# Kernel optimization log

Measured on AMD Instinct MI355X. Metric: run time of the kernel, lower is better.

The kernel has to match this reference:

```python
import jax, jax.numpy as jnp
import numpy as np

N_Q, N_X, N_Z = 1024, 512, 512
N_PER = N_Q + N_X + N_Z        # 2048 nodes per graph
B = 16                          # graphs per batch
DEG = 16                        # avg in/out degree
E_PER = N_PER * DEG
N = B * N_PER                   # 32768 total nodes
E = B * E_PER                   # 524288 total edges
HID, HEADS, L = 128, 4, 3
DH = HID // HEADS               # 32 per-head dim
EPS = 1e-5


def setup_inputs() -> dict:
    key = jax.random.key(0)
    ks = jax.random.split(key, 10)
    # one-hot node-type features (qubit / X-stab / Z-stab), tiled over batch
    sn = jnp.zeros((N_PER, 3), jnp.float32)
    sn = sn.at[:N_Q, 0].set(1.0).at[N_Q:N_Q + N_X, 1].set(1.0).at[N_Q + N_X:, 2].set(1.0)
    x = jnp.tile(sn, (B, 1))  # [N,3]
    # random sparse edges, graph-local then offset (mimics dense_to_sparse + Batch)
    src = jax.random.randint(ks[0], (B, E_PER), 0, N_PER)
    dst = jax.random.randint(ks[1], (B, E_PER), 0, N_PER)
    off = (jnp.arange(B) * N_PER)[:, None]
    edge_src = (src + off).reshape(-1).astype(jnp.int32)
    edge_dst = (dst + off).reshape(-1).astype(jnp.int32)
    seg = jnp.repeat(jnp.arange(B, dtype=jnp.int32), N_PER)  # graph id per node
    s = 0.05
    return dict(
        x=x, edge_src=edge_src, edge_dst=edge_dst, seg=seg,
        in_w=jax.random.normal(ks[2], (3, HID)) * s, in_b=jnp.zeros((HID,)),
        qw=jax.random.normal(ks[3], (L, HID, HID)) * s, qb=jnp.zeros((L, HID)),
        kw=jax.random.normal(ks[4], (L, HID, HID)) * s, kb=jnp.zeros((L, HID)),
        vw=jax.random.normal(ks[5], (L, HID, HID)) * s, vb=jnp.zeros((L, HID)),
        sw=jax.random.normal(ks[6], (L, HID, HID)) * s, sb=jnp.zeros((L, HID)),
        fw=jax.random.normal(ks[7], (L, HID, HID)) * s, fb=jnp.zeros((L, HID)),
        ln_g=jnp.ones((L, HID)), ln_b=jnp.zeros((L, HID)),
    )


def _layer_norm(h, g, b):
    mu = jnp.mean(h, axis=-1, keepdims=True)
    var = jnp.mean(jnp.square(h - mu), axis=-1, keepdims=True)
    return (h - mu) * jax.lax.rsqrt(var + EPS) * g + b


def reference(x, edge_src, edge_dst, seg, in_w, in_b, qw, qb, kw, kb, vw, vb,
              sw, sb, fw, fb, ln_g, ln_b):
    scale = 1.0 / jnp.sqrt(jnp.float32(DH))
    h = x @ in_w + in_b  # [N,HID]
    for i in range(L):
        h_res = h
        # TransformerConv: per-edge multi-head attention (softmax over in-neighbors)
        q = (h @ qw[i] + qb[i]).reshape(N, HEADS, DH)
        k = (h @ kw[i] + kb[i]).reshape(N, HEADS, DH)
        v = (h @ vw[i] + vb[i]).reshape(N, HEADS, DH)
        logits = jnp.einsum('ehd,ehd->eh', q[edge_dst], k[edge_src]) * scale  # [E,H]
        m = jax.ops.segment_max(logits, edge_dst, num_segments=N)             # [N,H]
        e = jnp.exp(logits - m[edge_dst])
        z = jax.ops.segment_sum(e, edge_dst, num_segments=N)                  # [N,H]
        alpha = e / z[edge_dst]
        agg = jax.ops.segment_sum(alpha[:, :, None] * v[edge_src], edge_dst,
                                  num_segments=N).reshape(N, HID)
        h = agg + h @ sw[i] + sb[i]        # root/skip linear (root_weight=True)
        # dropout is a no-op in eval mode
        h = h + jax.nn.relu(h @ fw[i] + fb[i])   # FFN residual
        h = h + h_res                            # outer residual
        h = jax.nn.relu(_layer_norm(h, ln_g[i], ln_b[i]))
    # global_mean_pool over graphs
    tot = jax.ops.segment_sum(h, seg, num_segments=B)                       # [B,HID]
    cnt = jax.ops.segment_sum(jnp.ones((N, 1), h.dtype), seg, num_segments=B)
    return tot / cnt
```

## Files before the change

### kernel.cpp

```cpp
#include <hip/hip_runtime.h>
#include <hip/hip_bf16.h>

#define N_TOT 32768
#define E_TOT 524288
#define HID 128
#define B_GR 16
#define NPER 2048
#define LAYERS 3
#define EPSLN 1e-5f
#define ELLW 64

typedef float f4 __attribute__((ext_vector_type(4)));
typedef float f2 __attribute__((ext_vector_type(2)));
typedef short bf16x8 __attribute__((ext_vector_type(8)));
typedef unsigned short u16x4 __attribute__((ext_vector_type(4)));

__device__ __forceinline__ unsigned short f2bf_rne(float x) {
    unsigned u = __float_as_uint(x);
    unsigned r = (u + 0x7FFFu + ((u >> 16) & 1u)) >> 16;
    return (unsigned short)r;
}

__device__ __forceinline__ void unpack8(uint4 w, float* f) {
    f[0] = __uint_as_float(w.x << 16); f[1] = __uint_as_float(w.x & 0xFFFF0000u);
    f[2] = __uint_as_float(w.y << 16); f[3] = __uint_as_float(w.y & 0xFFFF0000u);
    f[4] = __uint_as_float(w.z << 16); f[5] = __uint_as_float(w.z & 0xFFFF0000u);
    f[6] = __uint_as_float(w.w << 16); f[7] = __uint_as_float(w.w & 0xFFFF0000u);
}

__global__ __launch_bounds__(256) void k_zp(const float* __restrict__ qw, const float* __restrict__ kw,
                                            const float* __restrict__ vw, const float* __restrict__ sw,
                                            const float* __restrict__ fw, unsigned short* __restrict__ wt,
                                            int* __restrict__ cursor) {
    if (blockIdx.x < 960) {
        int mid = blockIdx.x >> 6;
        int within = (blockIdx.x & 63) * 256 + threadIdx.x;
        int l = mid / 5, t = mid % 5;
        const float* src = (t == 0 ? qw : t == 1 ? kw : t == 2 ? vw : t == 3 ? sw : fw) + l * HID * HID;
        int c = within >> 7;
        int kk = within & 127;
        int k = kk ^ ((c & 7) << 3);
        wt[mid * HID * HID + c * HID + kk] = f2bf_rne(src[k * HID + c]);
    } else {
        int i = (blockIdx.x - 960) * 256 + threadIdx.x;
        reinterpret_cast<int4*>(cursor)[i] = int4{0, 0, 0, 0};
    }
}

__global__ __launch_bounds__(256) void k_scatter_ell(const int* __restrict__ src, const int* __restrict__ dst,
                                                     int* __restrict__ cursor, int* __restrict__ ell) {
    int e = blockIdx.x * 256 + threadIdx.x;
    if (e < E_TOT) {
        int d = dst[e];
        int pos = atomicAdd(&cursor[d], 1);
        if (pos < ELLW) ell[d * ELLW + pos] = src[e];
    }
}

__device__ __forceinline__ void stage_A(const float* __restrict__ A, int r0,
                                        unsigned short (*A_lds)[HID], int tid) {
    #pragma unroll
    for (int p = 0; p < 8; ++p) {
        int idx = p * 256 + tid;
        int row = idx >> 5;
        int k0 = (idx & 31) * 4;
        f4 v = reinterpret_cast<const f4*>(A + (size_t)r0 * HID)[idx];
        u16x4 b = {f2bf_rne(v.x), f2bf_rne(v.y), f2bf_rne(v.z), f2bf_rne(v.w)};
        *reinterpret_cast<u16x4*>(&A_lds[row][k0 ^ ((row & 7) << 3)]) = b;
    }
}

#define GEMM_COMPUTE(acc, AL)                                                               \
    {                                                                                       \
        _Pragma("unroll")                                                                   \
        for (int ks = 0; ks < 4; ++ks) {                                                    \
            bf16x8 a0 = *reinterpret_cast<const bf16x8*>(                                   \
                &AL[wm * 32 + lr][(ks * 32 + lg * 8) ^ swz]);                               \
            bf16x8 a1 = *reinterpret_cast<const bf16x8*>(                                   \
                &AL[wm * 32 + 16 + lr][(ks * 32 + lg * 8) ^ swz]);                          \
            _Pragma("unroll")                                                               \
            for (int n = 0; n < 4; ++n) {                                                   \
                bf16x8 b = *reinterpret_cast<const bf16x8*>(                                \
                    &W_lds[wn * 64 + n * 16 + lr][(ks * 32 + lg * 8) ^ swz]);               \
                acc[0][n] = __builtin_amdgcn_mfma_f32_16x16x32_bf16(a0, b, acc[0][n], 0, 0, 0); \
                acc[1][n] = __builtin_amdgcn_mfma_f32_16x16x32_bf16(a1, b, acc[1][n], 0, 0, 0); \
            }                                                                               \
        }                                                                                   \
    }

__global__ __launch_bounds__(256) void k_init_qkv(const float* __restrict__ x,
                                                  const float* __restrict__ in_w,
                                                  const float* __restrict__ in_b,
                                                  const unsigned short* __restrict__ wl,
                                                  const float* __restrict__ qb, const float* __restrict__ kb,
                                                  const float* __restrict__ vb,
                                                  float* __restrict__ h,
                                                  unsigned short* __restrict__ oq, unsigned short* __restrict__ ok,
                                                  unsigned short* __restrict__ ov) {
    __shared__ unsigned short A_lds[64][HID];
    __shared__ unsigned short W_lds[HID][HID];
    int tid = threadIdx.x;
    int r0 = blockIdx.x * 64;
    int lane = tid & 63, w = tid >> 6;
    int wm = w >> 1, wn = w & 1;
    int lr = lane & 15, lg = lane >> 4;
    int swz = (lane & 7) << 3;

    #pragma unroll
    for (int p = 0; p < 8; ++p) {
        int idx = p * 256 + tid;
        int row = idx >> 5;
        int k0 = (idx & 31) * 4;
        int n = r0 + row;
        float x0 = x[n * 3 + 0], x1 = x[n * 3 + 1], x2 = x[n * 3 + 2];
        f4 o;
        #pragma unroll
        for (int i = 0; i < 4; ++i) {
            int c = k0 + i;
            o[i] = x0 * in_w[c] + x1 * in_w[HID + c] + x2 * in_w[2 * HID + c] + in_b[c];
        }
        reinterpret_cast<f4*>(h + (size_t)r0 * HID)[idx] = o;
        u16x4 b = {f2bf_rne(o[0]), f2bf_rne(o[1]), f2bf_rne(o[2]), f2bf_rne(o[3])};
        *reinterpret_cast<u16x4*>(&A_lds[row][k0 ^ ((row & 7) << 3)]) = b;
    }

    const float* biases[3] = {qb, kb, vb};
    unsigned short* outs[3] = {oq, ok, ov};
    #pragma unroll
    for (int t = 0; t < 3; ++t) {
        const unsigned short* Wp = wl + t * HID * HID;
        #pragma unroll
        for (int p = 0; p < 8; ++p) {
            int idx = p * 256 + tid;
            reinterpret_cast<f4*>(&W_lds[0][0])[idx] = reinterpret_cast<const f4*>(Wp)[idx];
        }
        __syncthreads();
        f4 acc[2][4];
        #pragma unroll
        for (int m = 0; m < 2; ++m)
            #pragma unroll
            for (int n = 0; n < 4; ++n) acc[m][n] = f4{0, 0, 0, 0};
        GEMM_COMPUTE(acc, A_lds);
        #pragma unroll
        for (int n = 0; n < 4; ++n) {
            int col = wn * 64 + n * 16 + lr;
            float bs = biases[t][col];
            #pragma unroll
            for (int m = 0; m < 2; ++m) {
                #pragma unroll
                for (int r = 0; r < 4; ++r) {
                    int row = r0 + wm * 32 + m * 16 + lg * 4 + r;
                    outs[t][(size_t)row * HID + col] = f2bf_rne(acc[m][n][r] + bs);
                }
            }
        }
        __syncthreads();
    }
}

__global__ __launch_bounds__(256) void k_attn4(const unsigned short* __restrict__ qb16,
                                               const unsigned short* __restrict__ kb16,
                                               const unsigned short* __restrict__ vb16,
                                               const int* __restrict__ deg,
                                               const int* __restrict__ ell,
                                               float* __restrict__ outagg) {
    int bid = blockIdx.x;
    int xcd = bid & 7;
    int chunk = bid >> 3;
    int g2 = xcd + 8 * (chunk >> 9);
    int nb = g2 * 512 + (chunk & 511);
    int n = nb * 4 + (threadIdx.x >> 6);

    int lane = threadIdx.x & 63;
    int g = lane >> 4, l = lane & 15;
    int dg = deg[n];
    if (dg > ELLW) dg = ELLW;
    const int base = n * ELLW;
    const float scale = 0.17677669529663687f;

    float qf[8];
    {
        uint4 qw = *reinterpret_cast<const uint4*>(&qb16[(size_t)n * HID + l * 8]);
        unpack8(qw, qf);
        #pragma unroll
        for (int c = 0; c < 8; ++c) qf[c] *= scale;
    }

    float z = 0.f;
    float a[8] = {0, 0, 0, 0, 0, 0, 0, 0};
    int nit = (dg + 3) >> 2;
    if (nit > 0) {
        int j = g;
        bool val = j < dg;
        int sj = ell[base + (val ? j : 0)];
        uint4 kw = *reinterpret_cast<const uint4*>(&kb16[(size_t)sj * HID + l * 8]);
        uint4 vw = *reinterpret_cast<const uint4*>(&vb16[(size_t)sj * HID + l * 8]);
        for (int it = 0; it < nit; ++it) {
            int jn = j + 4;
            bool valn = jn < dg;
            int sn = ell[base + (valn ? jn : 0)];
            uint4 kwn = *reinterpret_cast<const uint4*>(&kb16[(size_t)sn * HID + l * 8]);
            uint4 vwn = *reinterpret_cast<const uint4*>(&vb16[(size_t)sn * HID + l * 8]);
            float kf[8]; unpack8(kw, kf);
            float d = qf[0] * kf[0] + qf[1] * kf[1] + qf[2] * kf[2] + qf[3] * kf[3] +
                      qf[4] * kf[4] + qf[5] * kf[5] + qf[6] * kf[6] + qf[7] * kf[7];
            d += __shfl_xor(d, 1);
            d += __shfl_xor(d, 2);
            float p = val ? __expf(d) : 0.f;
            z += p;
            float vf[8]; unpack8(vw, vf);
            #pragma unroll
            for (int c = 0; c < 8; ++c) a[c] += p * vf[c];
            kw = kwn; vw = vwn; j = jn; val = valn;
        }
    }
    #pragma unroll
    for (int off = 16; off <= 32; off <<= 1) {
        z += __shfl_xor(z, off);
        #pragma unroll
        for (int c = 0; c < 8; ++c) a[c] += __shfl_xor(a[c], off);
    }
    if (g == 0) {
        float inv = (z > 0.f) ? 1.f / z : 0.f;
        f4 o0 = {a[0] * inv, a[1] * inv, a[2] * inv, a[3] * inv};
        f4 o1 = {a[4] * inv, a[5] * inv, a[6] * inv, a[7] * inv};
        f4* op = reinterpret_cast<f4*>(&outagg[(size_t)n * HID + l * 8]);
        op[0] = o0; op[1] = o1;
    }
}

template <bool QKV>
__global__ __launch_bounds__(256) void k_fused(const float* __restrict__ h,
                                               const unsigned short* __restrict__ wsf,
                                               const float* __restrict__ sb,
                                               const float* __restrict__ fb,
                                               const float* __restrict__ agg,
                                               const float* __restrict__ gma,
                                               const float* __restrict__ beta,
                                               float* __restrict__ out,
                                               const unsigned short* __restrict__ wqkv,
                                               const float* __restrict__ qb2,
                                               const float* __restrict__ kb2,
                                               const float* __restrict__ vb2,
                                               unsigned short* __restrict__ oq,
                                               unsigned short* __restrict__ ok,
                                               unsigned short* __restrict__ ov) {
    __shared__ __align__(16) char smem[50432];
    unsigned short (*A_lds)[HID] = reinterpret_cast<unsigned short (*)[HID]>(smem);
    unsigned short (*W_lds)[HID] = reinterpret_cast<unsigned short (*)[HID]>(smem + 16384);
    float (*T)[133] = reinterpret_cast<float (*)[133]>(smem + 16384);

    int tid = threadIdx.x;
    int r0 = blockIdx.x * 64;
    int lane = tid & 63, w = tid >> 6;
    int wm = w >> 1, wn = w & 1;
    int lr = lane & 15, lg = lane >> 4;
    int swz = (lane & 7) << 3;

    stage_A(h, r0, A_lds, tid);
    #pragma unroll
    for (int p = 0; p < 8; ++p) {
        int idx = p * 256 + tid;
        reinterpret_cast<f4*>(&W_lds[0][0])[idx] = reinterpret_cast<const f4*>(wsf)[idx];
    }
    __syncthreads();
    f4 acc[2][4];
    #pragma unroll
    for (int m = 0; m < 2; ++m)
        #pragma unroll
        for (int n = 0; n < 4; ++n) acc[m][n] = f4{0, 0, 0, 0};
    GEMM_COMPUTE(acc, A_lds);
    __syncthreads();

    #pragma unroll
    for (int n = 0; n < 4; ++n) {
        int col = wn * 64 + n * 16 + lr;
        float bs = sb[col];
        #pragma unroll
        for (int m = 0; m < 2; ++m) {
            #pragma unroll
            for (int r = 0; r < 4; ++r) {
                int rl = wm * 32 + m * 16 + lg * 4 + r;
                float v = acc[m][n][r] + bs + agg[(size_t)(r0 + rl) * HID + col];
                acc[m][n][r] = v;
                A_lds[rl][col ^ ((rl & 7) << 3)] = f2bf_rne(v);
            }
        }
    }
    #pragma unroll
    for (int p = 0; p < 8; ++p) {
        int idx = p * 256 + tid;
        reinterpret_cast<f4*>(&W_lds[0][0])[idx] = reinterpret_cast<const f4*>(wsf + HID * HID)[idx];
    }
    __syncthreads();
    f4 acc2[2][4];
    #pragma unroll
    for (int m = 0; m < 2; ++m)
        #pragma unroll
        for (int n = 0; n < 4; ++n) acc2[m][n] = f4{0, 0, 0, 0};
    GEMM_COMPUTE(acc2, A_lds);
    __syncthreads();

    #pragma unroll
    for (int n = 0; n < 4; ++n) {
        int col = wn * 64 + n * 16 + lr;
        float bs = fb[col];
        #pragma unroll
        for (int m = 0; m < 2; ++m) {
            #pragma unroll
            for (int r = 0; r < 4; ++r) {
                int rl = wm * 32 + m * 16 + lg * 4 + r;
                float t = acc[m][n][r] + fmaxf(acc2[m][n][r] + bs, 0.f) +
                          h[(size_t)(r0 + rl) * HID + col];
                T[rl][col] = t;
            }
        }
    }
    __syncthreads();

    int row = tid >> 2, qd = tid & 3;
    float s = 0.f, ss = 0.f;
    #pragma unroll 8
    for (int cc = 0; cc < 32; ++cc) {
        int c = (cc + qd * 8) & 31;
        float x = T[row][qd * 32 + c];
        s += x; ss += x * x;
    }
    s += __shfl_xor(s, 1);  s += __shfl_xor(s, 2);
    ss += __shfl_xor(ss, 1); ss += __shfl_xor(ss, 2);
    float mu = s * (1.f / 128.f);
    float var = ss * (1.f / 128.f) - mu * mu;
    float rsq = rsqrtf(fmaxf(var, 0.f) + EPSLN);
    int rswz = (row & 7) << 3;
    #pragma unroll
    for (int c4 = 0; c4 < 8; ++c4) {
        int cb = ((c4 + qd * 2) & 7) * 4;
        int col = qd * 32 + cb;
        f4 o;
        #pragma unroll
        for (int i = 0; i < 4; ++i) {
            float x = T[row][col + i];
            float y = (x - mu) * rsq * gma[col + i] + beta[col + i];
            o[i] = fmaxf(y, 0.f);
        }
        *reinterpret_cast<f4*>(&out[(size_t)(r0 + row) * HID + col]) = o;
        if (QKV) {
            u16x4 b = {f2bf_rne(o[0]), f2bf_rne(o[1]), f2bf_rne(o[2]), f2bf_rne(o[3])};
            *reinterpret_cast<u16x4*>(&A_lds[row][col ^ rswz]) = b;
        }
    }

    if (QKV) {
        __syncthreads();
        const float* biases[3] = {qb2, kb2, vb2};
        unsigned short* outs[3] = {oq, ok, ov};
        #pragma unroll
        for (int t = 0; t < 3; ++t) {
            const unsigned short* Wp = wqkv + t * HID * HID;
            #pragma unroll
            for (int p = 0; p < 8; ++p) {
                int idx = p * 256 + tid;
                reinterpret_cast<f4*>(&W_lds[0][0])[idx] = reinterpret_cast<const f4*>(Wp)[idx];
            }
            __syncthreads();
            f4 acc3[2][4];
            #pragma unroll
            for (int m = 0; m < 2; ++m)
                #pragma unroll
                for (int n = 0; n < 4; ++n) acc3[m][n] = f4{0, 0, 0, 0};
            GEMM_COMPUTE(acc3, A_lds);
            #pragma unroll
            for (int n = 0; n < 4; ++n) {
                int col = wn * 64 + n * 16 + lr;
                float bs = biases[t][col];
                #pragma unroll
                for (int m = 0; m < 2; ++m) {
                    #pragma unroll
                    for (int r = 0; r < 4; ++r) {
                        int rw = r0 + wm * 32 + m * 16 + lg * 4 + r;
                        outs[t][(size_t)rw * HID + col] = f2bf_rne(acc3[m][n][r] + bs);
                    }
                }
            }
            __syncthreads();
        }
    }
}

__global__ __launch_bounds__(128) void k_pool1(const float* __restrict__ h, float* __restrict__ partial) {
    int g = blockIdx.x >> 4, chunk = blockIdx.x & 15;
    int c = threadIdx.x;
    int n0 = g * NPER + chunk * 128;
    float s = 0.f;
    #pragma unroll 4
    for (int i = 0; i < 128; ++i) s += h[(size_t)(n0 + i) * HID + c];
    partial[(size_t)blockIdx.x * HID + c] = s;
}

__global__ __launch_bounds__(128) void k_pool2(const float* __restrict__ partial, float* __restrict__ out) {
    int g = blockIdx.x;
    int c = threadIdx.x;
    float s = 0.f;
    #pragma unroll
    for (int i = 0; i < 16; ++i) s += partial[(size_t)(g * 16 + i) * HID + c];
    out[g * HID + c] = s * (1.f / NPER);
}

extern "C" void kernel_launch(void* const* d_in, const int* in_sizes, int n_in,
                              void* d_out, int out_size, void* d_ws, size_t ws_size,
                              hipStream_t stream) {
    const float* x    = (const float*)d_in[0];
    const int*   esrc = (const int*)d_in[1];
    const int*   edst = (const int*)d_in[2];
    const float* in_w = (const float*)d_in[4];
    const float* in_b = (const float*)d_in[5];
    const float* qw   = (const float*)d_in[6];
    const float* qb   = (const float*)d_in[7];
    const float* kw   = (const float*)d_in[8];
    const float* kb   = (const float*)d_in[9];
    const float* vw   = (const float*)d_in[10];
    const float* vb   = (const float*)d_in[11];
    const float* sw   = (const float*)d_in[12];
    const float* sb   = (const float*)d_in[13];
    const float* fw   = (const float*)d_in[14];
    const float* fb   = (const float*)d_in[15];
    const float* ln_g = (const float*)d_in[16];
    const float* ln_b = (const float*)d_in[17];
    float* out = (float*)d_out;

    const size_t NH = (size_t)N_TOT * HID;
    float* h     = (float*)d_ws;
    float* t_buf = h + NH;
    float* partial = h + 2 * NH;
    unsigned short* qb16 = (unsigned short*)(partial + 256 * HID);
    unsigned short* kb16 = qb16 + NH;
    unsigned short* vb16 = kb16 + NH;
    unsigned short* wt   = vb16 + NH;
    int* cursor = (int*)(wt + 15 * HID * HID);
    int* ell    = cursor + N_TOT;

    k_zp<<<992, 256, 0, stream>>>(qw, kw, vw, sw, fw, wt, cursor);
    k_scatter_ell<<<E_TOT / 256, 256, 0, stream>>>(esrc, edst, cursor, ell);
    k_init_qkv<<<N_TOT / 64, 256, 0, stream>>>(x, in_w, in_b, wt, qb, kb, vb,
                                               h, qb16, kb16, vb16);

    for (int l = 0; l < LAYERS; ++l) {
        const unsigned short* wt_l = wt + (size_t)l * 5 * HID * HID;
        k_attn4<<<N_TOT / 4, 256, 0, stream>>>(qb16, kb16, vb16, cursor, ell, t_buf);
        if (l + 1 < LAYERS) {
            const unsigned short* wt_n = wt + (size_t)(l + 1) * 5 * HID * HID;
            k_fused<true><<<N_TOT / 64, 256, 0, stream>>>(
                h, wt_l + 3 * HID * HID, sb + (size_t)l * HID, fb + (size_t)l * HID,
                t_buf, ln_g + (size_t)l * HID, ln_b + (size_t)l * HID, h,
                wt_n, qb + (size_t)(l + 1) * HID, kb + (size_t)(l + 1) * HID,
                vb + (size_t)(l + 1) * HID, qb16, kb16, vb16);
        } else {
            k_fused<false><<<N_TOT / 64, 256, 0, stream>>>(
                h, wt_l + 3 * HID * HID, sb + (size_t)l * HID, fb + (size_t)l * HID,
                t_buf, ln_g + (size_t)l * HID, ln_b + (size_t)l * HID, h,
                nullptr, nullptr, nullptr, nullptr, nullptr, nullptr, nullptr);
        }
    }
    k_pool1<<<B_GR * 16, 128, 0, stream>>>(h, partial);
    k_pool2<<<B_GR, 128, 0, stream>>>(partial, out);
}
```

Measured before the change: 190.3 us.

## Interleave K/V, bf16 aggregates, 16-bit ELL indices, fold scale and pooling into kernels

```diff
diff --git a/kernel.cpp b/kernel.cpp
--- a/kernel.cpp
+++ b/kernel.cpp
@@ -9,9 +9,9 @@
 #define LAYERS 3
 #define EPSLN 1e-5f
 #define ELLW 64
+#define SCALE 0.17677669529663687f
 
 typedef float f4 __attribute__((ext_vector_type(4)));
-typedef float f2 __attribute__((ext_vector_type(2)));
 typedef short bf16x8 __attribute__((ext_vector_type(8)));
 typedef unsigned short u16x4 __attribute__((ext_vector_type(4)));
 
@@ -19,6 +19,10 @@
     unsigned u = __float_as_uint(x);
     unsigned r = (u + 0x7FFFu + ((u >> 16) & 1u)) >> 16;
     return (unsigned short)r;
+}
+
+__device__ __forceinline__ float bf2f(unsigned short u) {
+    return __uint_as_float(((unsigned)u) << 16);
 }
 
 __device__ __forceinline__ void unpack8(uint4 w, float* f) {
@@ -31,7 +35,7 @@
 __global__ __launch_bounds__(256) void k_zp(const float* __restrict__ qw, const float* __restrict__ kw,
                                             const float* __restrict__ vw, const float* __restrict__ sw,
                                             const float* __restrict__ fw, unsigned short* __restrict__ wt,
-                                            int* __restrict__ cursor) {
+                                            int* __restrict__ cursor, float* __restrict__ outz) {
     if (blockIdx.x < 960) {
         int mid = blockIdx.x >> 6;
         int within = (blockIdx.x & 63) * 256 + threadIdx.x;
@@ -40,20 +44,25 @@
         int c = within >> 7;
         int kk = within & 127;
         int k = kk ^ ((c & 7) << 3);
-        wt[mid * HID * HID + c * HID + kk] = f2bf_rne(src[k * HID + c]);
-    } else {
+        float sc = (t == 0) ? SCALE : 1.0f;
+        wt[mid * HID * HID + c * HID + kk] = f2bf_rne(src[k * HID + c] * sc);
+    } else if (blockIdx.x < 992) {
         int i = (blockIdx.x - 960) * 256 + threadIdx.x;
         reinterpret_cast<int4*>(cursor)[i] = int4{0, 0, 0, 0};
+    } else {
+        f4 z4 = {0.f, 0.f, 0.f, 0.f};
+        reinterpret_cast<f4*>(outz)[threadIdx.x * 2] = z4;
+        reinterpret_cast<f4*>(outz)[threadIdx.x * 2 + 1] = z4;
     }
 }
 
 __global__ __launch_bounds__(256) void k_scatter_ell(const int* __restrict__ src, const int* __restrict__ dst,
-                                                     int* __restrict__ cursor, int* __restrict__ ell) {
+                                                     int* __restrict__ cursor, unsigned short* __restrict__ ell) {
     int e = blockIdx.x * 256 + threadIdx.x;
     if (e < E_TOT) {
         int d = dst[e];
         int pos = atomicAdd(&cursor[d], 1);
-        if (pos < ELLW) ell[d * ELLW + pos] = src[e];
+        if (pos < ELLW) ell[d * ELLW + pos] = (unsigned short)src[e];
     }
 }
 
@@ -88,6 +97,26 @@
         }                                                                                   \
     }
 
+#define QKV_EPILOGUE(ACC, T_IDX)                                                            \
+    {                                                                                       \
+        _Pragma("unroll")                                                                   \
+        for (int n = 0; n < 4; ++n) {                                                       \
+            int col = wn * 64 + n * 16 + lr;                                                \
+            float bs = biases[T_IDX][col];                                                  \
+            if (T_IDX == 0) bs *= SCALE;                                                    \
+            unsigned short* outp = (T_IDX == 0) ? oq : okv + ((T_IDX == 2) ? 128 : 0);      \
+            const size_t stride = (T_IDX == 0) ? HID : 256;                                 \
+            _Pragma("unroll")                                                               \
+            for (int m = 0; m < 2; ++m) {                                                   \
+                _Pragma("unroll")                                                           \
+                for (int r = 0; r < 4; ++r) {                                               \
+                    int row = r0 + wm * 32 + m * 16 + lg * 4 + r;                           \
+                    outp[(size_t)row * stride + col] = f2bf_rne(ACC[m][n][r] + bs);         \
+                }                                                                           \
+            }                                                                               \
+        }                                                                                   \
+    }
+
 __global__ __launch_bounds__(256) void k_init_qkv(const float* __restrict__ x,
                                                   const float* __restrict__ in_w,
                                                   const float* __restrict__ in_b,
@@ -95,8 +124,8 @@
                                                   const float* __restrict__ qb, const float* __restrict__ kb,
                                                   const float* __restrict__ vb,
                                                   float* __restrict__ h,
-                                                  unsigned short* __restrict__ oq, unsigned short* __restrict__ ok,
-                                                  unsigned short* __restrict__ ov) {
+                                                  unsigned short* __restrict__ oq,
+                                                  unsigned short* __restrict__ okv) {
     __shared__ unsigned short A_lds[64][HID];
     __shared__ unsigned short W_lds[HID][HID];
     int tid = threadIdx.x;
@@ -125,7 +154,6 @@
     }
 
     const float* biases[3] = {qb, kb, vb};
-    unsigned short* outs[3] = {oq, ok, ov};
     #pragma unroll
     for (int t = 0; t < 3; ++t) {
         const unsigned short* Wp = wl + t * HID * HID;
@@ -141,29 +169,16 @@
             #pragma unroll
             for (int n = 0; n < 4; ++n) acc[m][n] = f4{0, 0, 0, 0};
         GEMM_COMPUTE(acc, A_lds);
-        #pragma unroll
-        for (int n = 0; n < 4; ++n) {
-            int col = wn * 64 + n * 16 + lr;
-            float bs = biases[t][col];
-            #pragma unroll
-            for (int m = 0; m < 2; ++m) {
-                #pragma unroll
-                for (int r = 0; r < 4; ++r) {
-                    int row = r0 + wm * 32 + m * 16 + lg * 4 + r;
-                    outs[t][(size_t)row * HID + col] = f2bf_rne(acc[m][n][r] + bs);
-                }
-            }
-        }
+        QKV_EPILOGUE(acc, t);
         __syncthreads();
     }
 }
 
-__global__ __launch_bounds__(256) void k_attn4(const unsigned short* __restrict__ qb16,
-                                               const unsigned short* __restrict__ kb16,
-                                               const unsigned short* __restrict__ vb16,
+__global__ __launch_bounds__(256) void k_attn5(const unsigned short* __restrict__ qb16,
+                                               const unsigned short* __restrict__ kv16,
                                                const int* __restrict__ deg,
-                                               const int* __restrict__ ell,
-                                               float* __restrict__ outagg) {
+                                               const unsigned short* __restrict__ ell,
+                                               unsigned short* __restrict__ outagg) {
     int bid = blockIdx.x;
     int xcd = bid & 7;
     int chunk = bid >> 3;
@@ -175,15 +190,12 @@
     int g = lane >> 4, l = lane & 15;
     int dg = deg[n];
     if (dg > ELLW) dg = ELLW;
-    const int base = n * ELLW;
-    const float scale = 0.17677669529663687f;
+    const unsigned short* eb = ell + n * ELLW;
 
     float qf[8];
     {
         uint4 qw = *reinterpret_cast<const uint4*>(&qb16[(size_t)n * HID + l * 8]);
         unpack8(qw, qf);
-        #pragma unroll
-        for (int c = 0; c < 8; ++c) qf[c] *= scale;
     }
 
     float z = 0.f;
@@ -192,15 +204,17 @@
     if (nit > 0) {
         int j = g;
         bool val = j < dg;
-        int sj = ell[base + (val ? j : 0)];
-        uint4 kw = *reinterpret_cast<const uint4*>(&kb16[(size_t)sj * HID + l * 8]);
-        uint4 vw = *reinterpret_cast<const uint4*>(&vb16[(size_t)sj * HID + l * 8]);
+        int sj = val ? (int)eb[j] : 0;
+        const unsigned short* kv = kv16 + (size_t)sj * 256 + l * 8;
+        uint4 kw = *reinterpret_cast<const uint4*>(kv);
+        uint4 vw = *reinterpret_cast<const uint4*>(kv + 128);
         for (int it = 0; it < nit; ++it) {
             int jn = j + 4;
             bool valn = jn < dg;
-            int sn = ell[base + (valn ? jn : 0)];
-            uint4 kwn = *reinterpret_cast<const uint4*>(&kb16[(size_t)sn * HID + l * 8]);
-            uint4 vwn = *reinterpret_cast<const uint4*>(&vb16[(size_t)sn * HID + l * 8]);
+            int sn = valn ? (int)eb[jn] : 0;
+            const unsigned short* kvn = kv16 + (size_t)sn * 256 + l * 8;
+            uint4 kwn = *reinterpret_cast<const uint4*>(kvn);
+            uint4 vwn = *reinterpret_cast<const uint4*>(kvn + 128);
             float kf[8]; unpack8(kw, kf);
             float d = qf[0] * kf[0] + qf[1] * kf[1] + qf[2] * kf[2] + qf[3] * kf[3] +
                       qf[4] * kf[4] + qf[5] * kf[5] + qf[6] * kf[6] + qf[7] * kf[7];
@@ -222,10 +236,12 @@
     }
     if (g == 0) {
         float inv = (z > 0.f) ? 1.f / z : 0.f;
-        f4 o0 = {a[0] * inv, a[1] * inv, a[2] * inv, a[3] * inv};
-        f4 o1 = {a[4] * inv, a[5] * inv, a[6] * inv, a[7] * inv};
-        f4* op = reinterpret_cast<f4*>(&outagg[(size_t)n * HID + l * 8]);
-        op[0] = o0; op[1] = o1;
+        uint4 o;
+        o.x = (unsigned)f2bf_rne(a[0] * inv) | ((unsigned)f2bf_rne(a[1] * inv) << 16);
+        o.y = (unsigned)f2bf_rne(a[2] * inv) | ((unsigned)f2bf_rne(a[3] * inv) << 16);
+        o.z = (unsigned)f2bf_rne(a[4] * inv) | ((unsigned)f2bf_rne(a[5] * inv) << 16);
+        o.w = (unsigned)f2bf_rne(a[6] * inv) | ((unsigned)f2bf_rne(a[7] * inv) << 16);
+        *reinterpret_cast<uint4*>(&outagg[(size_t)n * HID + l * 8]) = o;
     }
 }
 
@@ -234,7 +250,7 @@
                                                const unsigned short* __restrict__ wsf,
                                                const float* __restrict__ sb,
                                                const float* __restrict__ fb,
-                                               const float* __restrict__ agg,
+                                               const unsigned short* __restrict__ agg16,
                                                const float* __restrict__ gma,
                                                const float* __restrict__ beta,
                                                float* __restrict__ out,
@@ -243,8 +259,8 @@
                                                const float* __restrict__ kb2,
                                                const float* __restrict__ vb2,
                                                unsigned short* __restrict__ oq,
-                                               unsigned short* __restrict__ ok,
-                                               unsigned short* __restrict__ ov) {
+                                               unsigned short* __restrict__ okv,
+                                               float* __restrict__ pool_out) {
     __shared__ __align__(16) char smem[50432];
     unsigned short (*A_lds)[HID] = reinterpret_cast<unsigned short (*)[HID]>(smem);
     unsigned short (*W_lds)[HID] = reinterpret_cast<unsigned short (*)[HID]>(smem + 16384);
@@ -281,7 +297,7 @@
             #pragma unroll
             for (int r = 0; r < 4; ++r) {
                 int rl = wm * 32 + m * 16 + lg * 4 + r;
-                float v = acc[m][n][r] + bs + agg[(size_t)(r0 + rl) * HID + col];
+                float v = acc[m][n][r] + bs + bf2f(agg16[(size_t)(r0 + rl) * HID + col]);
                 acc[m][n][r] = v;
                 A_lds[rl][col ^ ((rl & 7) << 3)] = f2bf_rne(v);
             }
@@ -343,17 +359,19 @@
             float y = (x - mu) * rsq * gma[col + i] + beta[col + i];
             o[i] = fmaxf(y, 0.f);
         }
-        *reinterpret_cast<f4*>(&out[(size_t)(r0 + row) * HID + col]) = o;
         if (QKV) {
+            *reinterpret_cast<f4*>(&out[(size_t)(r0 + row) * HID + col]) = o;
             u16x4 b = {f2bf_rne(o[0]), f2bf_rne(o[1]), f2bf_rne(o[2]), f2bf_rne(o[3])};
             *reinterpret_cast<u16x4*>(&A_lds[row][col ^ rswz]) = b;
+        } else {
+            #pragma unroll
+            for (int i = 0; i < 4; ++i) T[row][col + i] = o[i];
         }
     }
 
     if (QKV) {
         __syncthreads();
         const float* biases[3] = {qb2, kb2, vb2};
-        unsigned short* outs[3] = {oq, ok, ov};
         #pragma unroll
         for (int t = 0; t < 3; ++t) {
             const unsigned short* Wp = wqkv + t * HID * HID;
@@ -369,41 +387,18 @@
                 #pragma unroll
                 for (int n = 0; n < 4; ++n) acc3[m][n] = f4{0, 0, 0, 0};
             GEMM_COMPUTE(acc3, A_lds);
-            #pragma unroll
-            for (int n = 0; n < 4; ++n) {
-                int col = wn * 64 + n * 16 + lr;
-                float bs = biases[t][col];
-                #pragma unroll
-                for (int m = 0; m < 2; ++m) {
-                    #pragma unroll
-                    for (int r = 0; r < 4; ++r) {
-                        int rw = r0 + wm * 32 + m * 16 + lg * 4 + r;
-                        outs[t][(size_t)rw * HID + col] = f2bf_rne(acc3[m][n][r] + bs);
-                    }
-                }
-            }
+            QKV_EPILOGUE(acc3, t);
             __syncthreads();
         }
-    }
-}
-
-__global__ __launch_bounds__(128) void k_pool1(const float* __restrict__ h, float* __restrict__ partial) {
-    int g = blockIdx.x >> 4, chunk = blockIdx.x & 15;
-    int c = threadIdx.x;
-    int n0 = g * NPER + chunk * 128;
-    float s = 0.f;
-    #pragma unroll 4
-    for (int i = 0; i < 128; ++i) s += h[(size_t)(n0 + i) * HID + c];
-    partial[(size_t)blockIdx.x * HID + c] = s;
-}
-
-__global__ __launch_bounds__(128) void k_pool2(const float* __restrict__ partial, float* __restrict__ out) {
-    int g = blockIdx.x;
-    int c = threadIdx.x;
-    float s = 0.f;
-    #pragma unroll
-    for (int i = 0; i < 16; ++i) s += partial[(size_t)(g * 16 + i) * HID + c];
-    out[g * HID + c] = s * (1.f / NPER);
+    } else {
+        __syncthreads();
+        if (tid < HID) {
+            float s2 = 0.f;
+            #pragma unroll 8
+            for (int r = 0; r < 64; ++r) s2 += T[r][tid];
+            atomicAdd(&pool_out[(r0 >> 11) * HID + tid], s2 * (1.f / NPER));
+        }
+    }
 }
 
 extern "C" void kernel_launch(void* const* d_in, const int* in_sizes, int n_in,
@@ -429,38 +424,34 @@
     float* out = (float*)d_out;
 
     const size_t NH = (size_t)N_TOT * HID;
-    float* h     = (float*)d_ws;
-    float* t_buf = h + NH;
-    float* partial = h + 2 * NH;
-    unsigned short* qb16 = (unsigned short*)(partial + 256 * HID);
-    unsigned short* kb16 = qb16 + NH;
-    unsigned short* vb16 = kb16 + NH;
-    unsigned short* wt   = vb16 + NH;
+    float* h = (float*)d_ws;
+    unsigned short* agg16 = (unsigned short*)(h + NH);
+    unsigned short* qb16  = agg16 + NH;
+    unsigned short* kv16  = qb16 + NH;
+    unsigned short* wt    = kv16 + 2 * NH;
     int* cursor = (int*)(wt + 15 * HID * HID);
-    int* ell    = cursor + N_TOT;
-
-    k_zp<<<992, 256, 0, stream>>>(qw, kw, vw, sw, fw, wt, cursor);
+    unsigned short* ell = (unsigned short*)(cursor + N_TOT);
+
+    k_zp<<<993, 256, 0, stream>>>(qw, kw, vw, sw, fw, wt, cursor, out);
     k_scatter_ell<<<E_TOT / 256, 256, 0, stream>>>(esrc, edst, cursor, ell);
     k_init_qkv<<<N_TOT / 64, 256, 0, stream>>>(x, in_w, in_b, wt, qb, kb, vb,
-                                               h, qb16, kb16, vb16);
+                                               h, qb16, kv16);
 
     for (int l = 0; l < LAYERS; ++l) {
         const unsigned short* wt_l = wt + (size_t)l * 5 * HID * HID;
-        k_attn4<<<N_TOT / 4, 256, 0, stream>>>(qb16, kb16, vb16, cursor, ell, t_buf);
+        k_attn5<<<N_TOT / 4, 256, 0, stream>>>(qb16, kv16, cursor, ell, agg16);
         if (l + 1 < LAYERS) {
             const unsigned short* wt_n = wt + (size_t)(l + 1) * 5 * HID * HID;
             k_fused<true><<<N_TOT / 64, 256, 0, stream>>>(
                 h, wt_l + 3 * HID * HID, sb + (size_t)l * HID, fb + (size_t)l * HID,
-                t_buf, ln_g + (size_t)l * HID, ln_b + (size_t)l * HID, h,
+                agg16, ln_g + (size_t)l * HID, ln_b + (size_t)l * HID, h,
                 wt_n, qb + (size_t)(l + 1) * HID, kb + (size_t)(l + 1) * HID,
-                vb + (size_t)(l + 1) * HID, qb16, kb16, vb16);
+                vb + (size_t)(l + 1) * HID, qb16, kv16, nullptr);
         } else {
             k_fused<false><<<N_TOT / 64, 256, 0, stream>>>(
                 h, wt_l + 3 * HID * HID, sb + (size_t)l * HID, fb + (size_t)l * HID,
-                t_buf, ln_g + (size_t)l * HID, ln_b + (size_t)l * HID, h,
-                nullptr, nullptr, nullptr, nullptr, nullptr, nullptr, nullptr);
-        }
-    }
-    k_pool1<<<B_GR * 16, 128, 0, stream>>>(h, partial);
-    k_pool2<<<B_GR, 128, 0, stream>>>(partial, out);
-}
+                agg16, ln_g + (size_t)l * HID, ln_b + (size_t)l * HID, h,
+                nullptr, nullptr, nullptr, nullptr, nullptr, nullptr, out);
+        }
+    }
+}
```

Result: faster. 172.4 us (-9.4%).
